# Kernel tuning notes

Measured on AMD Instinct MI355X. Metric: run time of the kernel, lower is better.

The kernel has to match this reference:

```python
import jax, jax.numpy as jnp
import numpy as np

C, T, D = 32, 768, 100      # n_countries, n_times, n_ages (=n_features)
H = 5                        # attention heads (EncoderLayer default)
HID_GCN = 60                 # GCN hidden features
FFN = 64                     # feed_forward_dim
NPRED = 10                   # n_predictions
LHID = 200                   # hid_linear_part_dim
NL = 3                       # encoder layers


def setup_inputs() -> dict:
    key = jax.random.key(0)
    ks = jax.random.split(key, 24)
    s = 0.05
    rn = lambda k, shp: jax.random.normal(k, shp, jnp.float32) * s
    return {
        "X": jax.random.normal(ks[0], (C, T, D), jnp.float32),
        "A": jax.random.uniform(ks[1], (C, C), jnp.float32),
        # GCN params
        "gcn_w1": rn(ks[2], (D, HID_GCN)),
        "gcn_b1": rn(ks[3], (HID_GCN,)),
        "gcn_w2": rn(ks[4], (HID_GCN, D)),
        "gcn_b2": rn(ks[5], (D,)),
        # 3 stacked encoder layers
        "enc_wq": rn(ks[6], (NL, H, D, D)),
        "enc_wk": rn(ks[7], (NL, H, D, D)),
        "enc_wv": rn(ks[8], (NL, H, D, D)),
        "enc_wm": rn(ks[9], (NL, H * D, D)),
        "enc_f1w": rn(ks[10], (NL, D, FFN)),
        "enc_f1b": rn(ks[11], (NL, FFN)),
        "enc_f2w": rn(ks[12], (NL, FFN, D)),
        "enc_f2b": rn(ks[13], (NL, D)),
        "enc_ln1g": jnp.ones((NL, D), jnp.float32),
        "enc_ln1b": jnp.zeros((NL, D), jnp.float32),
        "enc_ln2g": jnp.ones((NL, D), jnp.float32),
        "enc_ln2b": jnp.zeros((NL, D), jnp.float32),
        "lin1_w": rn(ks[14], (D, LHID)),
        "lin1_b": rn(ks[15], (LHID,)),
        "lin2_w": rn(ks[16], (LHID, D)),
        "lin2_b": rn(ks[17], (D,)),
    }


def _layer_norm(x, g, b, eps=1e-5):
    m = x.mean(-1, keepdims=True)
    v = ((x - m) ** 2).mean(-1, keepdims=True)
    return (x - m) / jnp.sqrt(v + eps) * g + b


def _encoder_layer(x, wq, wk, wv, wm, f1w, f1b, f2w, f2b, g1, b1, g2, b2):
    # x: [C, T, D]; wq/wk/wv: [H, D, D]
    Q = jnp.einsum('ctd,hde->chte', x, wq)
    K = jnp.einsum('ctd,hde->chte', x, wk)
    V = jnp.einsum('ctd,hde->chte', x, wv)
    scores = jnp.einsum('chte,chse->chts', Q, K) / jnp.sqrt(jnp.float32(D))
    attn = jax.nn.softmax(scores, axis=-1)
    out = jnp.einsum('chts,chse->chte', attn, V)        # [C,H,T,D]
    out = out.transpose(0, 2, 1, 3).reshape(x.shape[0], x.shape[1], H * D)
    x = _layer_norm(x + out @ wm, g1, b1)
    ffn = jax.nn.relu(x @ f1w + f1b) @ f2w + f2b
    return _layer_norm(x + ffn, g2, b2)


def reference(X, A, gcn_w1, gcn_b1, gcn_w2, gcn_b2,
              enc_wq, enc_wk, enc_wv, enc_wm,
              enc_f1w, enc_f1b, enc_f2w, enc_f2b,
              enc_ln1g, enc_ln1b, enc_ln2g, enc_ln2b,
              lin1_w, lin1_b, lin2_w, lin2_b):
    n = A.shape[0]
    adj = A + jnp.eye(n, dtype=A.dtype)
    adj_hat = adj / adj.sum(-1, keepdims=True)
    # GCN layer 1
    h = jnp.einsum('ij,jta->ita', adj_hat, X)
    h = jnp.einsum('ita,ao->ito', h, gcn_w1) + gcn_b1
    h = jax.nn.relu(h)
    # GCN layer 2
    h = jnp.einsum('ij,jta->ita', adj_hat, h)
    h = jnp.einsum('ita,ao->ito', h, gcn_w2) + gcn_b2
    # 3 encoder layers (fixed structural loop)
    for l in range(NL):
        h = _encoder_layer(h, enc_wq[l], enc_wk[l], enc_wv[l], enc_wm[l],
                           enc_f1w[l], enc_f1b[l], enc_f2w[l], enc_f2b[l],
                           enc_ln1g[l], enc_ln1b[l], enc_ln2g[l], enc_ln2b[l])
    last = h[:, -1, :]  # [C, D]
    def step(carry, _):
        p = (carry @ lin1_w + lin1_b) @ lin2_w + lin2_b
        return p, p
    _, preds = jax.lax.scan(step, last, None, length=NPRED)  # [NPRED, C, D]
    return preds.transpose(1, 0, 2)  # [C, NPRED, D]
```

## Files before the change

kernel.cpp:

```cpp
#include <hip/hip_runtime.h>


#define ROWS 24576

#define OFF_ADJ   0L
#define OFF_X0    1024L
#define OFF_X1    (OFF_X0 + 2457600L)
#define OFF_XROW  (OFF_X1 + 3932160L)
#define OFF_XT    (OFF_XROW + 1572864L)
#define OFF_WBF   (OFF_XT + 1572864L)
#define OFF_MHT   (OFF_WBF + 6291456L)
#define OFF_USTT  (OFF_MHT + 122880L)
#define OFF_MP    (OFF_USTT + 98304L)
#define OFF_C0    (OFF_MP + 10000L)
#define OFF_F1WT  (OFF_C0 + 128L)
#define OFF_F2WT  (OFF_F1WT + 12288L)
#define OFF_GW1T  (OFF_F2WT + 10752L)
#define OFF_GW2T  (OFF_GW1T + 4096L)

typedef __attribute__((ext_vector_type(8))) short short8;
typedef __attribute__((ext_vector_type(4))) float float4v;
typedef __attribute__((ext_vector_type(2))) unsigned int uint2v;

__device__ inline unsigned short f2bf(float f) {
    unsigned u = __builtin_bit_cast(unsigned, f);
    return (unsigned short)((u + 0x7fffu + ((u >> 16) & 1u)) >> 16);
}
__device__ inline unsigned pk2bf(float lo, float hi) {
    return (unsigned)f2bf(lo) | ((unsigned)f2bf(hi) << 16);
}
__device__ inline float bf2f(unsigned short v) {
    return __builtin_bit_cast(float, ((unsigned)v) << 16);
}
__device__ inline void gload16(const short* g, short* l) {
    __builtin_amdgcn_global_load_lds((const __attribute__((address_space(1))) void*)g,
                                     (__attribute__((address_space(3))) void*)l, 16, 0, 0);
}

__global__ void __launch_bounds__(256) k_mu2(const float* __restrict__ wq, const float* __restrict__ wk,
                                             const float* __restrict__ wv, const float* __restrict__ wm,
                                             const float* __restrict__ l1w, const float* __restrict__ l1b,
                                             const float* __restrict__ l2w, const float* __restrict__ l2b,
                                             const float* __restrict__ f1w, const float* __restrict__ f2w,
                                             const float* __restrict__ A,
                                             const float* __restrict__ gw1, const float* __restrict__ gw2,
                                             unsigned short* __restrict__ MhT, unsigned short* __restrict__ UstT,
                                             float* __restrict__ Mp, float* __restrict__ c0v,
                                             unsigned short* __restrict__ f1wT, unsigned short* __restrict__ f2wT,
                                             float* __restrict__ adjh,
                                             unsigned short* __restrict__ gw1T, unsigned short* __restrict__ gw2T) {
    int bi = blockIdx.x, tid = threadIdx.x;
    if (bi < 480) {
        int mat = bi >> 4, sub = bi & 15;
        int mode = mat / 15, idx = mat % 15, l = idx / 5, h = idx % 5;
        const float* Asrc = (mode == 0 ? wq : wv) + (l*5 + h)*10000;
        const float* Bsrc = (mode == 0) ? (wk + (l*5 + h)*10000) : (wm + l*50000 + h*10000);
        int oend = sub*625 + 625;
        for (int o = sub*625 + tid; o < oend; o += 256) {
            int r = o / 100, cix = o - (o/100)*100;
            const float* arow = Asrc + r*100;
            float acc = 0.f;
            if (mode == 0) {
                const float* brow = Bsrc + cix*100;
                for (int e = 0; e < 100; ++e) acc += arow[e] * brow[e];
                MhT[(long)(l*5 + h)*16384 + cix*128 + r] = f2bf(acc * 0.1f);
            } else {
                for (int e = 0; e < 100; ++e) acc += arow[e] * Bsrc[e*100 + cix];
                UstT[(long)l*65536 + (long)cix*512 + h*100 + r] = f2bf(acc);
            }
        }
        if (sub == 0) {
            if (mode == 0) {
                unsigned short* M0 = MhT + (long)(l*5 + h)*16384;
                for (int i = tid; i < 28*128; i += 256) M0[(100 + i/128)*128 + (i%128)] = 0;
                for (int i = tid; i < 100*28; i += 256) M0[(i/28)*128 + 100 + (i%28)] = 0;
            } else if (h == 4) {
                unsigned short* U0 = UstT + (long)l*65536;
                for (int i = tid; i < 28*512; i += 256) U0[(long)(100 + i/512)*512 + (i%512)] = 0;
                for (int i = tid; i < 100*12; i += 256) U0[(long)(i/12)*512 + 500 + (i%12)] = 0;
            }
        }
    } else if (bi < 496) {
        int sub = bi - 480;
        int oend = sub*625 + 625;
        for (int o = sub*625 + tid; o < oend; o += 256) {
            int r = o / 100, cix = o - (o/100)*100;
            const float* arow = l1w + r*200;
            float acc = 0.f;
            for (int e = 0; e < 200; ++e) acc += arow[e] * l2w[e*100 + cix];
            Mp[r*100 + cix] = acc;
        }
    } else if (bi == 496) {
        if (tid < 100) {
            float acc = l2b[tid];
            for (int e = 0; e < 200; ++e) acc += l1b[e] * l2w[e*100 + tid];
            c0v[tid] = acc;
        }
    } else if (bi < 500) {
        int l = bi - 497;
        unsigned short* F1 = f1wT + (long)l*8192;
        for (int i = tid; i < 8192; i += 256) {
            int o = i >> 7, k = i & 127;
            F1[i] = (k < 100) ? f2bf(f1w[l*6400 + k*64 + o]) : (unsigned short)0;
        }
        unsigned short* F2 = f2wT + (long)l*7168;
        for (int i = tid; i < 7168; i += 256) {
            int o2 = i >> 6, k2 = i & 63;
            F2[i] = (o2 < 100) ? f2bf(f2w[l*6400 + k2*100 + o2]) : (unsigned short)0;
        }
    } else if (bi == 500) {
        __shared__ float adj[1024];
        __shared__ float rs[32];
        for (int i = tid; i < 1024; i += 256) {
            int r = i >> 5, j = i & 31;
            adj[i] = A[i] + (r == j ? 1.f : 0.f);
        }
        __syncthreads();
        if (tid < 32) {
            float s = 0.f;
            #pragma unroll
            for (int jj = 0; jj < 32; ++jj) s += adj[tid*32 + jj];
            rs[tid] = s;
        }
        __syncthreads();
        for (int i = tid; i < 1024; i += 256) adjh[i] = adj[i] / rs[i >> 5];
    } else {
        for (int i = tid; i < 8192; i += 256) {
            int o = i >> 7, k = i & 127;
            gw1T[i] = (o < 60 && k < 100) ? f2bf(gw1[k*60 + o]) : (unsigned short)0;
        }
        for (int i = tid; i < 7168; i += 256) {
            int o = i >> 6, k = i & 63;
            gw2T[i] = (o < 100 && k < 60) ? f2bf(gw2[k*100 + o]) : (unsigned short)0;
        }
    }
}

__global__ void __launch_bounds__(128) k_gw1(const float* __restrict__ X,
                                             const unsigned short* __restrict__ gw1T,
                                             unsigned short* __restrict__ g) {
    const int tid = threadIdx.x, wave = tid >> 6, lane = tid & 63;
    const int l15 = lane & 15, l4 = lane >> 4;
    const long row = (long)blockIdx.x*32 + wave*16 + l15;
    const float* xrp = X + row*100;
    float4v acc[4];
    #pragma unroll
    for (int mt = 0; mt < 4; ++mt) acc[mt] = (float4v){0,0,0,0};
    #pragma unroll
    for (int ks = 0; ks < 4; ++ks) {
        short8 b;
        #pragma unroll
        for (int e = 0; e < 8; ++e) {
            int k = ks*32 + l4*8 + e;
            b[e] = (k < 100) ? (short)f2bf(xrp[k]) : (short)0;
        }
        #pragma unroll
        for (int mt = 0; mt < 4; ++mt) {
            short8 a = *(const short8*)((const short*)gw1T + (mt*16 + l15)*128 + ks*32 + l4*8);
            acc[mt] = __builtin_amdgcn_mfma_f32_16x16x32_bf16(a, b, acc[mt], 0, 0, 0);
        }
    }
    #pragma unroll
    for (int mt = 0; mt < 4; ++mt) {
        int o0 = mt*16 + l4*4;
        *(uint2v*)(g + row*64 + o0) =
            (uint2v){pk2bf(acc[mt][0], acc[mt][1]), pk2bf(acc[mt][2], acc[mt][3])};
    }
}

__global__ void __launch_bounds__(256) k_spmmg(const float* __restrict__ adjh,
                                               const unsigned short* __restrict__ g,
                                               const float* __restrict__ b1,
                                               unsigned short* __restrict__ hid) {
    __shared__ float adj[1024];
    int tid = threadIdx.x;
    for (int i = tid; i < 1024; i += 256) adj[i] = adjh[i];
    __syncthreads();
    long p = (long)blockIdx.x*256 + tid;
    int o = (int)(p & 63);
    float acc[32];
    #pragma unroll
    for (int i = 0; i < 32; ++i) acc[i] = 0.f;
    for (int j = 0; j < 32; ++j) {
        float xv = bf2f(g[(long)j*49152 + p]);
        #pragma unroll
        for (int i = 0; i < 32; ++i) acc[i] += adj[i*32 + j] * xv;
    }
    float bias = (o < 60) ? b1[o] : 0.f;
    #pragma unroll
    for (int i = 0; i < 32; ++i) hid[(long)i*49152 + p] = f2bf(fmaxf(acc[i] + bias, 0.f));
}

__global__ void __launch_bounds__(128) k_gw2(const unsigned short* __restrict__ hid,
                                             const unsigned short* __restrict__ gw2T,
                                             unsigned short* __restrict__ h2) {
    const int tid = threadIdx.x, wave = tid >> 6, lane = tid & 63;
    const int l15 = lane & 15, l4 = lane >> 4;
    const long row = (long)blockIdx.x*32 + wave*16 + l15;
    float4v acc[7];
    #pragma unroll
    for (int mt = 0; mt < 7; ++mt) acc[mt] = (float4v){0,0,0,0};
    #pragma unroll
    for (int ks = 0; ks < 2; ++ks) {
        short8 b = *(const short8*)((const short*)hid + row*64 + ks*32 + l4*8);
        #pragma unroll
        for (int mt = 0; mt < 7; ++mt) {
            short8 a = *(const short8*)((const short*)gw2T + (mt*16 + l15)*64 + ks*32 + l4*8);
            acc[mt] = __builtin_amdgcn_mfma_f32_16x16x32_bf16(a, b, acc[mt], 0, 0, 0);
        }
    }
    #pragma unroll
    for (int mt = 0; mt < 7; ++mt) {
        int o0 = mt*16 + l4*4;
        *(uint2v*)(h2 + row*128 + o0) =
            (uint2v){pk2bf(acc[mt][0], acc[mt][1]), pk2bf(acc[mt][2], acc[mt][3])};
    }
    *(uint2v*)(h2 + row*128 + 112 + l4*4) = (uint2v){0u, 0u};
}

__global__ void __launch_bounds__(384) k_spmmx(const float* __restrict__ adjh,
                                               const unsigned short* __restrict__ h2,
                                               const float* __restrict__ b2,
                                               float* __restrict__ x0,
                                               unsigned short* __restrict__ xrow,
                                               unsigned short* __restrict__ xT) {
    __shared__ float adj[1024];
    int tid = threadIdx.x;
    for (int i = tid; i < 1024; i += 384) adj[i] = adjh[i];
    __syncthreads();
    long p = (long)blockIdx.x*384 + tid;
    int o = (int)(p & 127);
    int t = (int)(p >> 7);
    float acc[32];
    #pragma unroll
    for (int i = 0; i < 32; ++i) acc[i] = 0.f;
    for (int j = 0; j < 32; ++j) {
        float xv = bf2f(h2[(long)j*98304 + p]);
        #pragma unroll
        for (int i = 0; i < 32; ++i) acc[i] += adj[i*32 + j] * xv;
    }
    if (o < 100) {
        float bias = b2[o];
        #pragma unroll
        for (int i = 0; i < 32; ++i) {
            float v = acc[i] + bias;
            x0[((long)i*768 + t)*100 + o] = v;
            unsigned short bv = f2bf(v);
            xrow[((long)i*768 + t)*128 + o] = bv;
            xT[(long)i*98304 + (long)o*768 + t] = bv;
        }
    } else {
        #pragma unroll
        for (int i = 0; i < 32; ++i) {
            xrow[((long)i*768 + t)*128 + o] = 0;
            if (o < 112) xT[(long)i*98304 + (long)o*768 + t] = 0;
        }
    }
}

#define QP_STRIDE 136
#define PT_STRIDE 72

__global__ void __launch_bounds__(256) k_attn6(const unsigned short* __restrict__ xrow,
                                               const unsigned short* __restrict__ xT,
                                               const unsigned short* __restrict__ MhT,
                                               unsigned short* __restrict__ Wb) {
    __shared__ __align__(16) short xr[64 * 128];
    __shared__ __align__(16) short xt[112 * 64];
    __shared__ __align__(16) short scratch[4][2304];
    const int tid = threadIdx.x;
    const int wave = tid >> 6, lane = tid & 63;
    const int l15 = lane & 15, l4 = lane >> 4;
    const int c = blockIdx.z, h = blockIdx.y, q0 = blockIdx.x * 128;
    short* myq = scratch[wave];
    short* pt0 = scratch[wave];
    short* pt1 = scratch[wave] + 1152;

    short8 qb0[4], qb1[4];
    {
        const short* xq = (const short*)xrow + ((long)c*768 + q0 + wave*16 + l15)*128 + l4*8;
        short8 bq0[4], bq1[4];
        #pragma unroll
        for (int kk = 0; kk < 4; ++kk) {
            bq0[kk] = *(const short8*)(xq + kk*32);
            bq1[kk] = *(const short8*)(xq + 64*128 + kk*32);
        }
        const short* Mb = (const short*)MhT + (long)h*16384 + l15*128 + l4*8;
        float4v qc0[8], qc1[8];
        #pragma unroll
        for (int mt = 0; mt < 8; ++mt) { qc0[mt] = (float4v){0,0,0,0}; qc1[mt] = (float4v){0,0,0,0}; }
        #pragma unroll
        for (int mt = 0; mt < 8; ++mt) {
            #pragma unroll
            for (int kk = 0; kk < 4; ++kk) {
                short8 a = *(const short8*)(Mb + (mt*16)*128 + kk*32);
                qc0[mt] = __builtin_amdgcn_mfma_f32_16x16x32_bf16(a, bq0[kk], qc0[mt], 0, 0, 0);
                qc1[mt] = __builtin_amdgcn_mfma_f32_16x16x32_bf16(a, bq1[kk], qc1[mt], 0, 0, 0);
            }
        }
        #pragma unroll
        for (int mt = 0; mt < 8; ++mt)
            *(uint2v*)(myq + l15*QP_STRIDE + mt*16 + l4*4) =
                (uint2v){pk2bf(qc0[mt][0], qc0[mt][1]), pk2bf(qc0[mt][2], qc0[mt][3])};
        #pragma unroll
        for (int kk = 0; kk < 4; ++kk) qb0[kk] = *(const short8*)(myq + l15*QP_STRIDE + kk*32 + l4*8);
        #pragma unroll
        for (int mt = 0; mt < 8; ++mt)
            *(uint2v*)(myq + l15*QP_STRIDE + mt*16 + l4*4) =
                (uint2v){pk2bf(qc1[mt][0], qc1[mt][1]), pk2bf(qc1[mt][2], qc1[mt][3])};
        #pragma unroll
        for (int kk = 0; kk < 4; ++kk) qb1[kk] = *(const short8*)(myq + l15*QP_STRIDE + kk*32 + l4*8);
    }

    float4v o0[7], o1[7];
    #pragma unroll
    for (int n = 0; n < 7; ++n) { o0[n] = (float4v){0,0,0,0}; o1[n] = (float4v){0,0,0,0}; }
    float lsum0 = 0.f, lsum1 = 0.f;

    const short* xrg = (const short*)xrow + (long)c*768*128;
    const short* xtg = (const short*)xT + (long)c*128*768;
    const int rl4 = lane >> 4, cp16 = lane & 15;
    const int rl8 = lane >> 3, cp8 = lane & 7;
    const int njt = (wave == 3) ? 2 : 4;

    for (int kt = 0; kt < 12; ++kt) {
        const int key0 = kt * 64;
        #pragma unroll
        for (int j = 0; j < 4; ++j) {
            int row = wave*16 + j*4 + rl4;
            int lc = cp16 ^ (row & 7);
            gload16(xrg + (long)(key0 + row)*128 + lc*8, xr + (wave*16 + j*4)*128);
        }
        for (int j = 0; j < njt; ++j) {
            int row = wave*32 + j*8 + rl8;
            int lc = cp8 ^ (row & 7);
            gload16(xtg + (long)row*768 + key0 + lc*8, xt + (wave*32 + j*8)*64);
        }
        __syncthreads();

        float4v s0[4], s1[4];
        #pragma unroll
        for (int kn = 0; kn < 4; ++kn) { s0[kn] = (float4v){0,0,0,0}; s1[kn] = (float4v){0,0,0,0}; }
        #pragma unroll
        for (int kn = 0; kn < 4; ++kn) {
            #pragma unroll
            for (int kk = 0; kk < 4; ++kk) {
                short8 a = *(const short8*)(xr + (kn*16 + l15)*128 + (((kk*4 + l4) ^ (l15 & 7))*8));
                s0[kn] = __builtin_amdgcn_mfma_f32_16x16x32_bf16(a, qb0[kk], s0[kn], 0, 0, 0);
                s1[kn] = __builtin_amdgcn_mfma_f32_16x16x32_bf16(a, qb1[kk], s1[kn], 0, 0, 0);
            }
        }

        #pragma unroll
        for (int kn = 0; kn < 4; ++kn) {
            float p0[4], p1[4];
            #pragma unroll
            for (int r = 0; r < 4; ++r) {
                p0[r] = __expf(s0[kn][r]); lsum0 += p0[r];
                p1[r] = __expf(s1[kn][r]); lsum1 += p1[r];
            }
            *(uint2v*)(pt0 + l15*PT_STRIDE + kn*16 + l4*4) =
                (uint2v){pk2bf(p0[0], p0[1]), pk2bf(p0[2], p0[3])};
            *(uint2v*)(pt1 + l15*PT_STRIDE + kn*16 + l4*4) =
                (uint2v){pk2bf(p1[0], p1[1]), pk2bf(p1[2], p1[3])};
        }

        #pragma unroll
        for (int kk2 = 0; kk2 < 2; ++kk2) {
            short8 b0 = *(const short8*)(pt0 + l15*PT_STRIDE + kk2*32 + l4*8);
            short8 b1 = *(const short8*)(pt1 + l15*PT_STRIDE + kk2*32 + l4*8);
            #pragma unroll
            for (int dt = 0; dt < 7; ++dt) {
                short8 a = *(const short8*)(xt + (dt*16 + l15)*64 + (((kk2*4 + l4) ^ (l15 & 7))*8));
                o0[dt] = __builtin_amdgcn_mfma_f32_16x16x32_bf16(a, b0, o0[dt], 0, 0, 0);
                o1[dt] = __builtin_amdgcn_mfma_f32_16x16x32_bf16(a, b1, o1[dt], 0, 0, 0);
            }
        }
        __syncthreads();
    }

    float l0 = lsum0, l1 = lsum1;
    l0 += __shfl_xor(l0, 16, 64); l0 += __shfl_xor(l0, 32, 64);
    l1 += __shfl_xor(l1, 16, 64); l1 += __shfl_xor(l1, 32, 64);
    float inv0 = 1.f / l0, inv1 = 1.f / l1;

    unsigned short* Wo0 = Wb + ((long)(c*768 + q0 + wave*16 + l15))*512 + h*100 + l4*4;
    unsigned short* Wo1 = Wo0 + 64*512;
    #pragma unroll
    for (int dt = 0; dt < 7; ++dt) {
        if (dt < 6 || l4 == 0) {
            *(uint2v*)(Wo0 + dt*16) = (uint2v){pk2bf(o0[dt][0]*inv0, o0[dt][1]*inv0),
                                               pk2bf(o0[dt][2]*inv0, o0[dt][3]*inv0)};
            *(uint2v*)(Wo1 + dt*16) = (uint2v){pk2bf(o1[dt][0]*inv1, o1[dt][1]*inv1),
                                               pk2bf(o1[dt][2]*inv1, o1[dt][3]*inv1)};
        }
    }
    if (h == 0) {
        unsigned short* Wz = Wb + ((long)c*768 + q0)*512 + 500;
        for (int i = tid; i < 1536; i += 256) Wz[(long)(i/12)*512 + (i%12)] = 0;
    }
}

template<bool EMIT>
__global__ void __launch_bounds__(128) k_tail(const unsigned short* __restrict__ Wb,
        const unsigned short* __restrict__ UstT,
        const unsigned short* __restrict__ f1wT, const unsigned short* __restrict__ f2wT,
        const float* __restrict__ f1b, const float* __restrict__ f2b,
        const float* __restrict__ g1, const float* __restrict__ b1,
        const float* __restrict__ g2, const float* __restrict__ b2,
        float* __restrict__ x, unsigned short* __restrict__ xrow, unsigned short* __restrict__ xT) {
    __shared__ __align__(16) short zS[2][16*136];
    __shared__ __align__(16) short tS[2][16*72];
    const int tid = threadIdx.x, wave = tid >> 6, lane = tid & 63;
    const int l15 = lane & 15, l4 = lane >> 4;
    const long row = (long)blockIdx.x*32 + wave*16 + l15;
    const int cc = blockIdx.x / 24;
    const int tt = (blockIdx.x % 24)*32 + wave*16 + l15;
    short* myz = zS[wave];
    short* myt = tS[wave];

    const short* Wr = (const short*)Wb + row*512 + l4*8;
    float4v o[8];
    #pragma unroll
    for (int mt = 0; mt < 8; ++mt) o[mt] = (float4v){0,0,0,0};
    for (int ks = 0; ks < 16; ++ks) {
        short8 b = *(const short8*)(Wr + ks*32);
        #pragma unroll
        for (int mt = 0; mt < 8; ++mt) {
            short8 a = *(const short8*)((const short*)UstT + (long)(mt*16 + l15)*512 + ks*32 + l4*8);
            o[mt] = __builtin_amdgcn_mfma_f32_16x16x32_bf16(a, b, o[mt], 0, 0, 0);
        }
    }

    float zv[7][4];
    float sum = 0.f;
    #pragma unroll
    for (int mt = 0; mt < 7; ++mt) {
        int f0 = mt*16 + l4*4;
        float4 xv = {0,0,0,0};
        if (f0 < 100) xv = *(const float4*)(x + row*100 + f0);
        #pragma unroll
        for (int r = 0; r < 4; ++r) {
            float z = 0.f;
            if (f0 < 100) { z = o[mt][r] + ((const float*)&xv)[r]; sum += z; }
            zv[mt][r] = z;
        }
    }
    sum += __shfl_xor(sum, 16, 64); sum += __shfl_xor(sum, 32, 64);
    float mean = sum * 0.01f;
    float vs = 0.f;
    #pragma unroll
    for (int mt = 0; mt < 7; ++mt) {
        if (mt*16 + l4*4 < 100) {
            #pragma unroll
            for (int r = 0; r < 4; ++r) { float d = zv[mt][r] - mean; vs += d*d; }
        }
    }
    vs += __shfl_xor(vs, 16, 64); vs += __shfl_xor(vs, 32, 64);
    float inv = rsqrtf(vs * 0.01f + 1e-5f);
    float x1r[7][4];
    #pragma unroll
    for (int mt = 0; mt < 7; ++mt) {
        int f0 = mt*16 + l4*4;
        float4 gv = {0,0,0,0}, bv = {0,0,0,0};
        if (f0 < 100) { gv = *(const float4*)(g1 + f0); bv = *(const float4*)(b1 + f0); }
        #pragma unroll
        for (int r = 0; r < 4; ++r)
            x1r[mt][r] = (f0 < 100) ? (zv[mt][r] - mean) * inv * ((const float*)&gv)[r] + ((const float*)&bv)[r] : 0.f;
    }

    #pragma unroll
    for (int mt = 0; mt < 8; ++mt) {
        float v0 = (mt < 7) ? x1r[mt][0] : 0.f, v1 = (mt < 7) ? x1r[mt][1] : 0.f;
        float v2 = (mt < 7) ? x1r[mt][2] : 0.f, v3 = (mt < 7) ? x1r[mt][3] : 0.f;
        *(uint2v*)(myz + l15*136 + mt*16 + l4*4) = (uint2v){pk2bf(v0, v1), pk2bf(v2, v3)};
    }

    float4v t2[4];
    #pragma unroll
    for (int m2t = 0; m2t < 4; ++m2t) t2[m2t] = (float4v){0,0,0,0};
    #pragma unroll
    for (int ks = 0; ks < 4; ++ks) {
        short8 b = *(const short8*)(myz + l15*136 + ks*32 + l4*8);
        #pragma unroll
        for (int m2t = 0; m2t < 4; ++m2t) {
            short8 a = *(const short8*)((const short*)f1wT + (m2t*16 + l15)*128 + ks*32 + l4*8);
            t2[m2t] = __builtin_amdgcn_mfma_f32_16x16x32_bf16(a, b, t2[m2t], 0, 0, 0);
        }
    }
    #pragma unroll
    for (int m2t = 0; m2t < 4; ++m2t) {
        int m20 = m2t*16 + l4*4;
        float4 bv = *(const float4*)(f1b + m20);
        float v0 = fmaxf(t2[m2t][0] + ((const float*)&bv)[0], 0.f);
        float v1 = fmaxf(t2[m2t][1] + ((const float*)&bv)[1], 0.f);
        float v2 = fmaxf(t2[m2t][2] + ((const float*)&bv)[2], 0.f);
        float v3 = fmaxf(t2[m2t][3] + ((const float*)&bv)[3], 0.f);
        *(uint2v*)(myt + l15*72 + m20) = (uint2v){pk2bf(v0, v1), pk2bf(v2, v3)};
    }

    float4v o3[7];
    #pragma unroll
    for (int m3t = 0; m3t < 7; ++m3t) o3[m3t] = (float4v){0,0,0,0};
    #pragma unroll
    for (int ks2 = 0; ks2 < 2; ++ks2) {
        short8 b = *(const short8*)(myt + l15*72 + ks2*32 + l4*8);
        #pragma unroll
        for (int m3t = 0; m3t < 7; ++m3t) {
            short8 a = *(const short8*)((const short*)f2wT + (m3t*16 + l15)*64 + ks2*32 + l4*8);
            o3[m3t] = __builtin_amdgcn_mfma_f32_16x16x32_bf16(a, b, o3[m3t], 0, 0, 0);
        }
    }

    float z2[7][4];
    float sum2 = 0.f;
    #pragma unroll
    for (int m3t = 0; m3t < 7; ++m3t) {
        int f0 = m3t*16 + l4*4;
        float4 bv = {0,0,0,0};
        if (f0 < 100) bv = *(const float4*)(f2b + f0);
        #pragma unroll
        for (int r = 0; r < 4; ++r) {
            float z = 0.f;
            if (f0 < 100) { z = o3[m3t][r] + ((const float*)&bv)[r] + x1r[m3t][r]; sum2 += z; }
            z2[m3t][r] = z;
        }
    }
    sum2 += __shfl_xor(sum2, 16, 64); sum2 += __shfl_xor(sum2, 32, 64);
    float mean2 = sum2 * 0.01f;
    float vs2 = 0.f;
    #pragma unroll
    for (int m3t = 0; m3t < 7; ++m3t) {
        if (m3t*16 + l4*4 < 100) {
            #pragma unroll
            for (int r = 0; r < 4; ++r) { float d = z2[m3t][r] - mean2; vs2 += d*d; }
        }
    }
    vs2 += __shfl_xor(vs2, 16, 64); vs2 += __shfl_xor(vs2, 32, 64);
    float inv2 = rsqrtf(vs2 * 0.01f + 1e-5f);

    unsigned short* xTc = EMIT ? (xT + (long)cc*98304 + tt) : nullptr;
    #pragma unroll
    for (int m3t = 0; m3t < 7; ++m3t) {
        int f0 = m3t*16 + l4*4;
        if (f0 < 100) {
            float4 gv = *(const float4*)(g2 + f0);
            float4 bv = *(const float4*)(b2 + f0);
            float y[4];
            #pragma unroll
            for (int r = 0; r < 4; ++r)
                y[r] = (z2[m3t][r] - mean2) * inv2 * ((const float*)&gv)[r] + ((const float*)&bv)[r];
            *(float4*)(x + row*100 + f0) = (float4){y[0], y[1], y[2], y[3]};
            if (EMIT) {
                *(uint2v*)(xrow + row*128 + f0) = (uint2v){pk2bf(y[0], y[1]), pk2bf(y[2], y[3])};
                #pragma unroll
                for (int r = 0; r < 4; ++r)
                    xTc[(long)(f0 + r)*768] = f2bf(y[r]);
            }
        } else if (EMIT) {
            *(uint2v*)(xrow + row*128 + f0) = (uint2v){0u, 0u};
            #pragma unroll
            for (int r = 0; r < 4; ++r)
                if (f0 + r < 112) xTc[(long)(f0 + r)*768] = 0;
        }
    }
    if (EMIT) *(uint2v*)(xrow + row*128 + 112 + l4*4) = (uint2v){0u, 0u};
}

__global__ void __launch_bounds__(256) k_pred2(const float* __restrict__ xf,
        const float* __restrict__ Mp, const float* __restrict__ c0v,
        float* __restrict__ out) {
    int c = blockIdx.x, tid = threadIdx.x;
    __shared__ float Ml[10000];
    __shared__ float carry[100];
    for (int i = tid; i < 10000; i += 256) Ml[i] = Mp[i];
    if (tid < 100) carry[tid] = xf[((long)c*768 + 767)*100 + tid];
    __syncthreads();
    for (int s = 0; s < 10; ++s) {
        float pv = 0.f;
        if (tid < 100) {
            pv = c0v[tid];
            for (int d = 0; d < 100; ++d) pv += carry[d] * Ml[d*100 + tid];
            out[((long)c*10 + s)*100 + tid] = pv;
        }
        __syncthreads();
        if (tid < 100) carry[tid] = pv;
        __syncthreads();
    }
}

extern "C" void kernel_launch(void* const* d_in, const int* in_sizes, int n_in,
                              void* d_out, int out_size, void* d_ws, size_t ws_size,
                              hipStream_t stream) {
    const float* X    = (const float*)d_in[0];
    const float* A    = (const float*)d_in[1];
    const float* gw1  = (const float*)d_in[2];
    const float* gb1  = (const float*)d_in[3];
    const float* gw2  = (const float*)d_in[4];
    const float* gb2  = (const float*)d_in[5];
    const float* wq   = (const float*)d_in[6];
    const float* wk   = (const float*)d_in[7];
    const float* wv   = (const float*)d_in[8];
    const float* wm   = (const float*)d_in[9];
    const float* f1w  = (const float*)d_in[10];
    const float* f1b  = (const float*)d_in[11];
    const float* f2w  = (const float*)d_in[12];
    const float* f2b  = (const float*)d_in[13];
    const float* ln1g = (const float*)d_in[14];
    const float* ln1b = (const float*)d_in[15];
    const float* ln2g = (const float*)d_in[16];
    const float* ln2b = (const float*)d_in[17];
    const float* l1w  = (const float*)d_in[18];
    const float* l1b  = (const float*)d_in[19];
    const float* l2w  = (const float*)d_in[20];
    const float* l2b  = (const float*)d_in[21];
    (void)in_sizes; (void)n_in; (void)out_size; (void)ws_size;

    float* ws   = (float*)d_ws;
    float* adjh = ws + OFF_ADJ;
    float* x0   = ws + OFF_X0;
    unsigned short* gbuf = (unsigned short*)(ws + OFF_X1);
    unsigned short* hbuf = (unsigned short*)(ws + OFF_X1 + 786432L);
    unsigned short* h2buf= (unsigned short*)(ws + OFF_X1 + 1572864L);
    unsigned short* xrow = (unsigned short*)(ws + OFF_XROW);
    unsigned short* xTb  = (unsigned short*)(ws + OFF_XT);
    unsigned short* Wbf  = (unsigned short*)(ws + OFF_WBF);
    unsigned short* MhT  = (unsigned short*)(ws + OFF_MHT);
    unsigned short* UstT = (unsigned short*)(ws + OFF_USTT);
    float* Mp   = ws + OFF_MP;
    float* c0v  = ws + OFF_C0;
    unsigned short* f1wT = (unsigned short*)(ws + OFF_F1WT);
    unsigned short* f2wT = (unsigned short*)(ws + OFF_F2WT);
    unsigned short* gw1T = (unsigned short*)(ws + OFF_GW1T);
    unsigned short* gw2T = (unsigned short*)(ws + OFF_GW2T);
    float* out  = (float*)d_out;

    k_mu2<<<502, 256, 0, stream>>>(wq, wk, wv, wm, l1w, l1b, l2w, l2b, f1w, f2w, A, gw1, gw2,
                                   MhT, UstT, Mp, c0v, f1wT, f2wT, adjh, gw1T, gw2T);

    k_gw1<<<768, 128, 0, stream>>>(X, gw1T, gbuf);
    k_spmmg<<<192, 256, 0, stream>>>(adjh, gbuf, gb1, hbuf);
    k_gw2<<<768, 128, 0, stream>>>(hbuf, gw2T, h2buf);
    k_spmmx<<<256, 384, 0, stream>>>(adjh, h2buf, gb2, x0, xrow, xTb);

    for (int l = 0; l < 3; ++l) {
        k_attn6<<<dim3(6,5,32), 256, 0, stream>>>(xrow, xTb, MhT + (long)l*81920, Wbf);
        if (l < 2)
            k_tail<true><<<768, 128, 0, stream>>>(Wbf, UstT + (long)l*65536,
                f1wT + (long)l*8192, f2wT + (long)l*7168, f1b + l*64, f2b + l*100,
                ln1g + l*100, ln1b + l*100, ln2g + l*100, ln2b + l*100, x0, xrow, xTb);
        else
            k_tail<false><<<768, 128, 0, stream>>>(Wbf, UstT + (long)l*65536,
                f1wT + (long)l*8192, f2wT + (long)l*7168, f1b + l*64, f2b + l*100,
                ln1g + l*100, ln1b + l*100, ln2g + l*100, ln2b + l*100, x0, xrow, xTb);
    }

    k_pred2<<<32, 256, 0, stream>>>(x0, Mp, c0v, out);
}
```

Measured before the change: 531.3 us.

## Read attention K/V tiles directly from global and use hardware bf16 packing

The attention kernel no longer stages key and transposed-value tiles into shared memory with global_load_lds and a block barrier each iteration. MFMA operands are read straight from global memory, relying on L2/L1 caching, and shared memory is used only for per-wave Q and P scratch. Float-to-bf16 packing now uses the v_cvt_pk_bf16_f32 instruction instead of manual rounding, and compiler memory fences are added around LDS reuse. The risk is higher global load latency and uncoalesced reads in the inner loop, plus a leftover s_barrier per tile.

```diff
diff --git a/kernel.cpp b/kernel.cpp
--- a/kernel.cpp
+++ b/kernel.cpp
@@ -19,6 +19,7 @@
 #define OFF_GW2T  (OFF_GW1T + 4096L)
 
 typedef __attribute__((ext_vector_type(8))) short short8;
+typedef __attribute__((ext_vector_type(4))) short short4v;
 typedef __attribute__((ext_vector_type(4))) float float4v;
 typedef __attribute__((ext_vector_type(2))) unsigned int uint2v;
 
@@ -27,14 +28,15 @@
     return (unsigned short)((u + 0x7fffu + ((u >> 16) & 1u)) >> 16);
 }
 __device__ inline unsigned pk2bf(float lo, float hi) {
-    return (unsigned)f2bf(lo) | ((unsigned)f2bf(hi) << 16);
+    unsigned r;
+    asm("v_cvt_pk_bf16_f32 %0, %1, %2" : "=v"(r) : "v"(lo), "v"(hi));
+    return r;
+}
+__device__ inline void st4s(short* p, unsigned a, unsigned b) {
+    *(short4v*)p = __builtin_bit_cast(short4v, (uint2v){a, b});
 }
 __device__ inline float bf2f(unsigned short v) {
     return __builtin_bit_cast(float, ((unsigned)v) << 16);
-}
-__device__ inline void gload16(const short* g, short* l) {
-    __builtin_amdgcn_global_load_lds((const __attribute__((address_space(1))) void*)g,
-                                     (__attribute__((address_space(3))) void*)l, 16, 0, 0);
 }
 
 __global__ void __launch_bounds__(256) k_mu2(const float* __restrict__ wq, const float* __restrict__ wk,
@@ -261,20 +263,21 @@
 #define QP_STRIDE 136
 #define PT_STRIDE 72
 
-__global__ void __launch_bounds__(256) k_attn6(const unsigned short* __restrict__ xrow,
+__global__ void __launch_bounds__(256) k_attn9(const unsigned short* __restrict__ xrow,
                                                const unsigned short* __restrict__ xT,
                                                const unsigned short* __restrict__ MhT,
                                                unsigned short* __restrict__ Wb) {
-    __shared__ __align__(16) short xr[64 * 128];
-    __shared__ __align__(16) short xt[112 * 64];
-    __shared__ __align__(16) short scratch[4][2304];
+    __shared__ __align__(16) short scratch[4][4608];
     const int tid = threadIdx.x;
     const int wave = tid >> 6, lane = tid & 63;
     const int l15 = lane & 15, l4 = lane >> 4;
     const int c = blockIdx.z, h = blockIdx.y, q0 = blockIdx.x * 128;
     short* myq = scratch[wave];
-    short* pt0 = scratch[wave];
-    short* pt1 = scratch[wave] + 1152;
+    short* pt0 = scratch[wave] + 2304;
+    short* pt1 = scratch[wave] + 3456;
+
+    const short* xrg = (const short*)xrow + (long)c*768*128;
+    const short* xtg = (const short*)xT + (long)c*128*768;
 
     short8 qb0[4], qb1[4];
     {
@@ -300,43 +303,30 @@
         }
         #pragma unroll
         for (int mt = 0; mt < 8; ++mt)
-            *(uint2v*)(myq + l15*QP_STRIDE + mt*16 + l4*4) =
-                (uint2v){pk2bf(qc0[mt][0], qc0[mt][1]), pk2bf(qc0[mt][2], qc0[mt][3])};
+            st4s(myq + l15*QP_STRIDE + mt*16 + l4*4,
+                 pk2bf(qc0[mt][0], qc0[mt][1]), pk2bf(qc0[mt][2], qc0[mt][3]));
+        asm volatile("" ::: "memory");
         #pragma unroll
         for (int kk = 0; kk < 4; ++kk) qb0[kk] = *(const short8*)(myq + l15*QP_STRIDE + kk*32 + l4*8);
+        asm volatile("" ::: "memory");
         #pragma unroll
         for (int mt = 0; mt < 8; ++mt)
-            *(uint2v*)(myq + l15*QP_STRIDE + mt*16 + l4*4) =
-                (uint2v){pk2bf(qc1[mt][0], qc1[mt][1]), pk2bf(qc1[mt][2], qc1[mt][3])};
+            st4s(myq + l15*QP_STRIDE + mt*16 + l4*4,
+                 pk2bf(qc1[mt][0], qc1[mt][1]), pk2bf(qc1[mt][2], qc1[mt][3]));
+        asm volatile("" ::: "memory");
         #pragma unroll
         for (int kk = 0; kk < 4; ++kk) qb1[kk] = *(const short8*)(myq + l15*QP_STRIDE + kk*32 + l4*8);
     }
+
+    __syncthreads();
 
     float4v o0[7], o1[7];
     #pragma unroll
     for (int n = 0; n < 7; ++n) { o0[n] = (float4v){0,0,0,0}; o1[n] = (float4v){0,0,0,0}; }
     float lsum0 = 0.f, lsum1 = 0.f;
 
-    const short* xrg = (const short*)xrow + (long)c*768*128;
-    const short* xtg = (const short*)xT + (long)c*128*768;
-    const int rl4 = lane >> 4, cp16 = lane & 15;
-    const int rl8 = lane >> 3, cp8 = lane & 7;
-    const int njt = (wave == 3) ? 2 : 4;
-
     for (int kt = 0; kt < 12; ++kt) {
         const int key0 = kt * 64;
-        #pragma unroll
-        for (int j = 0; j < 4; ++j) {
-            int row = wave*16 + j*4 + rl4;
-            int lc = cp16 ^ (row & 7);
-            gload16(xrg + (long)(key0 + row)*128 + lc*8, xr + (wave*16 + j*4)*128);
-        }
-        for (int j = 0; j < njt; ++j) {
-            int row = wave*32 + j*8 + rl8;
-            int lc = cp8 ^ (row & 7);
-            gload16(xtg + (long)row*768 + key0 + lc*8, xt + (wave*32 + j*8)*64);
-        }
-        __syncthreads();
 
         float4v s0[4], s1[4];
         #pragma unroll
@@ -345,7 +335,7 @@
         for (int kn = 0; kn < 4; ++kn) {
             #pragma unroll
             for (int kk = 0; kk < 4; ++kk) {
-                short8 a = *(const short8*)(xr + (kn*16 + l15)*128 + (((kk*4 + l4) ^ (l15 & 7))*8));
+                short8 a = *(const short8*)(xrg + (long)(key0 + kn*16 + l15)*128 + kk*32 + l4*8);
                 s0[kn] = __builtin_amdgcn_mfma_f32_16x16x32_bf16(a, qb0[kk], s0[kn], 0, 0, 0);
                 s1[kn] = __builtin_amdgcn_mfma_f32_16x16x32_bf16(a, qb1[kk], s1[kn], 0, 0, 0);
             }
@@ -359,11 +349,13 @@
                 p0[r] = __expf(s0[kn][r]); lsum0 += p0[r];
                 p1[r] = __expf(s1[kn][r]); lsum1 += p1[r];
             }
-            *(uint2v*)(pt0 + l15*PT_STRIDE + kn*16 + l4*4) =
-                (uint2v){pk2bf(p0[0], p0[1]), pk2bf(p0[2], p0[3])};
-            *(uint2v*)(pt1 + l15*PT_STRIDE + kn*16 + l4*4) =
-                (uint2v){pk2bf(p1[0], p1[1]), pk2bf(p1[2], p1[3])};
-        }
+            st4s(pt0 + l15*PT_STRIDE + kn*16 + l4*4,
+                 pk2bf(p0[0], p0[1]), pk2bf(p0[2], p0[3]));
+            st4s(pt1 + l15*PT_STRIDE + kn*16 + l4*4,
+                 pk2bf(p1[0], p1[1]), pk2bf(p1[2], p1[3]));
+        }
+        asm volatile("" ::: "memory");
+        __builtin_amdgcn_s_barrier();
 
         #pragma unroll
         for (int kk2 = 0; kk2 < 2; ++kk2) {
@@ -371,7 +363,7 @@
             short8 b1 = *(const short8*)(pt1 + l15*PT_STRIDE + kk2*32 + l4*8);
             #pragma unroll
             for (int dt = 0; dt < 7; ++dt) {
-                short8 a = *(const short8*)(xt + (dt*16 + l15)*64 + (((kk2*4 + l4) ^ (l15 & 7))*8));
+                short8 a = *(const short8*)(xtg + (long)(dt*16 + l15)*768 + key0 + kk2*32 + l4*8);
                 o0[dt] = __builtin_amdgcn_mfma_f32_16x16x32_bf16(a, b0, o0[dt], 0, 0, 0);
                 o1[dt] = __builtin_amdgcn_mfma_f32_16x16x32_bf16(a, b1, o1[dt], 0, 0, 0);
             }
@@ -473,8 +465,9 @@
     for (int mt = 0; mt < 8; ++mt) {
         float v0 = (mt < 7) ? x1r[mt][0] : 0.f, v1 = (mt < 7) ? x1r[mt][1] : 0.f;
         float v2 = (mt < 7) ? x1r[mt][2] : 0.f, v3 = (mt < 7) ? x1r[mt][3] : 0.f;
-        *(uint2v*)(myz + l15*136 + mt*16 + l4*4) = (uint2v){pk2bf(v0, v1), pk2bf(v2, v3)};
-    }
+        st4s(myz + l15*136 + mt*16 + l4*4, pk2bf(v0, v1), pk2bf(v2, v3));
+    }
+    asm volatile("" ::: "memory");
 
     float4v t2[4];
     #pragma unroll
@@ -496,8 +489,9 @@
         float v1 = fmaxf(t2[m2t][1] + ((const float*)&bv)[1], 0.f);
         float v2 = fmaxf(t2[m2t][2] + ((const float*)&bv)[2], 0.f);
         float v3 = fmaxf(t2[m2t][3] + ((const float*)&bv)[3], 0.f);
-        *(uint2v*)(myt + l15*72 + m20) = (uint2v){pk2bf(v0, v1), pk2bf(v2, v3)};
-    }
+        st4s(myt + l15*72 + m20, pk2bf(v0, v1), pk2bf(v2, v3));
+    }
+    asm volatile("" ::: "memory");
 
     float4v o3[7];
     #pragma unroll
@@ -644,7 +638,7 @@
     k_spmmx<<<256, 384, 0, stream>>>(adjh, h2buf, gb2, x0, xrow, xTb);
 
     for (int l = 0; l < 3; ++l) {
-        k_attn6<<<dim3(6,5,32), 256, 0, stream>>>(xrow, xTb, MhT + (long)l*81920, Wbf);
+        k_attn9<<<dim3(6,5,32), 256, 0, stream>>>(xrow, xTb, MhT + (long)l*81920, Wbf);
         if (l < 2)
             k_tail<true><<<768, 128, 0, stream>>>(Wbf, UstT + (long)l*65536,
                 f1wT + (long)l*8192, f2wT + (long)l*7168, f1b + l*64, f2b + l*100,
```

New measurement: 884.7 us. 66.5% more time.
